# Kernel optimization log

Hardware: AMD Instinct MI355X
Metric: run time of the kernel (lower is better)

The kernel has to match this reference:

```python
import jax, jax.numpy as jnp
import numpy as np
import math

# irreps: 512x0 + 512x1 + 512x2 + 512x3 + 512x4 (SO3), mul_ir layout
LS = [0, 1, 2, 3, 4]
MULS = [512, 512, 512, 512, 512]
LMAX = 4
N = 4096
DIM = sum(m * (2 * l + 1) for m, l in zip(MULS, LS))  # 12800


def _small_d(l, beta):
    """Complex Wigner small-d matrix d^l_{m',m}(beta), m ordered -l..l (numpy, static)."""
    d = np.zeros((2 * l + 1, 2 * l + 1))
    cb, sb = math.cos(beta / 2.0), math.sin(beta / 2.0)
    for i, mp in enumerate(range(-l, l + 1)):
        for j, m in enumerate(range(-l, l + 1)):
            num = math.sqrt(math.factorial(l + mp) * math.factorial(l - mp)
                            * math.factorial(l + m) * math.factorial(l - m))
            tot = 0.0
            for s in range(max(0, m - mp), min(l + m, l - mp) + 1):
                den = (math.factorial(l + m - s) * math.factorial(s)
                       * math.factorial(mp - m + s) * math.factorial(l - mp - s))
                tot += ((-1.0) ** (mp - m + s)) * num / den \
                       * cb ** (2 * l + m - mp - 2 * s) * sb ** (mp - m + 2 * s)
            d[i, j] = tot
    return d


def _real_basis(l):
    """Unitary complex->real spherical-harmonic change of basis A (rows: real m=-l..l)."""
    A = np.zeros((2 * l + 1, 2 * l + 1), dtype=complex)
    A[l, l] = 1.0
    inv_s2 = 1.0 / math.sqrt(2.0)
    for m in range(1, l + 1):
        A[l + m, l + m] = ((-1) ** m) * inv_s2
        A[l + m, l - m] = inv_s2
        A[l - m, l + m] = -1j * ((-1) ** m) * inv_s2
        A[l - m, l - m] = 1j * inv_s2
    return A


def _J(l):
    """Real Wigner-D of the +pi/2 rotation that maps the 'easy' axis onto x.
    Conjugating the closed-form easy-axis rotation by J gives the x-axis rotation."""
    A = _real_basis(l)
    Dc = _small_d(l, math.pi / 2.0).astype(complex)
    return np.real(A @ Dc @ A.conj().T).astype(np.float32)


_JS = {l: _J(l) for l in LS if l > 0}


def _encode(angle, lmax):
    """[cos(l a), ..., cos(a), 1, sin(a), ..., sin(l a)] exactly as encode_rotation_angle."""
    m = jnp.arange(1, lmax + 1, dtype=angle.dtype)
    a = angle[:, None]
    c = jnp.cos(m * a)
    s = jnp.sin(m * a)
    return jnp.concatenate([c[:, ::-1], jnp.ones_like(a), s], axis=-1)  # [N, 2*lmax+1]


def _easy(enc, l, lmax):
    """Per-sample easy-axis rotation matrix for degree l built from the angle encoding.
    Rows/cols ordered m = -l..l: diag cos(|m|a), antidiag -sin(m a)."""
    d = 2 * l + 1
    m = np.arange(-l, l + 1)
    sign = np.sign(m).astype(np.float32)
    cos_v = enc[:, lmax - np.abs(m)]                 # [N, d] cos(|m| a)
    sin_v = enc[:, lmax + np.abs(m)] * sign          # [N, d] sin(m a)
    i = np.arange(d)
    E = jnp.zeros((enc.shape[0], d, d), enc.dtype)
    E = E.at[:, i, i].set(cos_v)
    E = E.at[:, i, d - 1 - i].add(-sin_v)            # add: center (m=0) overlaps diag, sin(0)=0
    return E


def _rotate(gamma, beta, alpha, x):
    n = x.shape[0]
    eg = _encode(gamma, LMAX)
    eb = _encode(beta, LMAX)
    ea = _encode(alpha, LMAX)
    outs = []
    off = 0
    for mul, l in zip(MULS, LS):
        d = 2 * l + 1
        seg = x[:, off:off + mul * d].reshape(n, mul, d)
        off += mul * d
        if l == 0:
            outs.append(seg.reshape(n, mul))  # scalars are rotation-invariant
            continue
        J = jnp.asarray(_JS[l], dtype=x.dtype)
        Eg = _easy(eg, l, LMAX)
        Eb = _easy(eb, l, LMAX)
        Ea = _easy(ea, l, LMAX)
        # yxy rotation: D = E(alpha) . J . E(beta) . J^T . E(gamma)
        D = Ea @ jnp.matmul(J, Eb @ jnp.matmul(J.T, Eg))  # [N, d, d]
        outs.append(jnp.einsum('nij,nuj->nui', D, seg).reshape(n, mul * d))
    return jnp.concatenate(outs, axis=-1)


def setup_inputs() -> dict:
    key = jax.random.key(0)
    kg, kb, ka, kx = jax.random.split(key, 4)
    pi = math.pi
    return {
        'gamma': jax.random.uniform(kg, (N,), jnp.float32, -pi, pi),
        'beta': jax.random.uniform(kb, (N,), jnp.float32, -pi, pi),
        'alpha': jax.random.uniform(ka, (N,), jnp.float32, -pi, pi),
        'x': jax.random.normal(kx, (N, DIM), jnp.float32),
    }


def reference(gamma, beta, alpha, x):
    return _rotate(gamma, beta, alpha, x)
```

## Files before the change

### kernel.cpp

```cpp
#include <hip/hip_runtime.h>
#include <math.h>

#define NSAMP 4096
#define DIMX  12800

#define JTOT 164

__global__ __launch_bounds__(256) void initJ_kernel(float* __restrict__ Jout) {
    __shared__ double dm[JTOT];
    __shared__ double Ar[JTOT], Ai[JTOT];
    __shared__ double Br[JTOT], Bi[JTOT];

    const int tid = threadIdx.x;
    int l = 0, base = 0, d = 0, ii = 0, jj = 0;
    const bool act = tid < JTOT;
    if (act) {
        if (tid < 9)       { l = 1; base = 0; }
        else if (tid < 34) { l = 2; base = 9; }
        else if (tid < 83) { l = 3; base = 34; }
        else               { l = 4; base = 83; }
        d = 2 * l + 1;
        int loc = tid - base;
        ii = loc / d;
        jj = loc - ii * d;

        double fact[9];
        fact[0] = 1.0;
        for (int k = 1; k < 9; k++) fact[k] = fact[k - 1] * (double)k;

        const int mp = ii - l, m = jj - l;
        const double num = sqrt(fact[l + mp] * fact[l - mp] * fact[l + m] * fact[l - m]);
        const double c2 = 0.70710678118654752440;
        double tot = 0.0;
        const int s0 = (m - mp > 0) ? (m - mp) : 0;
        const int s1 = (l + m < l - mp) ? (l + m) : (l - mp);
        for (int s = s0; s <= s1; s++) {
            double den = fact[l + m - s] * fact[s] * fact[mp - m + s] * fact[l - mp - s];
            int etot = (2 * l + m - mp - 2 * s) + (mp - m + 2 * s);
            double p = 1.0;
            for (int q = 0; q < etot; q++) p *= c2;
            double sgn = ((mp - m + s) & 1) ? -1.0 : 1.0;
            tot += sgn * (num / den) * p;
        }
        dm[tid] = tot;

        double ar = 0.0, ai = 0.0;
        const double inv_s2 = 0.70710678118654752440;
        if (ii == l) {
            if (jj == l) ar = 1.0;
        } else if (ii > l) {
            int mm = ii - l;
            if (jj == l + mm)      ar = (mm & 1) ? -inv_s2 : inv_s2;
            else if (jj == l - mm) ar = inv_s2;
        } else {
            int mm = l - ii;
            if (jj == l + mm)      ai = (mm & 1) ? inv_s2 : -inv_s2;
            else if (jj == l - mm) ai = inv_s2;
        }
        Ar[tid] = ar; Ai[tid] = ai;
    }
    __syncthreads();
    if (act) {
        double br = 0.0, bi = 0.0;
        for (int k = 0; k < d; k++) {
            double dv = dm[base + k * d + jj];
            br += Ar[base + ii * d + k] * dv;
            bi += Ai[base + ii * d + k] * dv;
        }
        Br[tid] = br; Bi[tid] = bi;
    }
    __syncthreads();
    if (act) {
        double jr = 0.0;
        for (int k = 0; k < d; k++) {
            jr += Br[base + ii * d + k] * Ar[base + jj * d + k]
                + Bi[base + ii * d + k] * Ai[base + jj * d + k];
        }
        Jout[tid] = (float)jr;
    }
}

template <int L>
__device__ __forceinline__ void apply_l(const float* __restrict__ xs_base,
                                        float* __restrict__ os_base,
                                        const float* __restrict__ Dl, int tid) {
    constexpr int d = 2 * L + 1;
#pragma unroll
    for (int rep = 0; rep < 2; rep++) {
        const int g = tid + rep * 256;
        const float* xs = xs_base + g * d;
        float v[d];
#pragma unroll
        for (int j = 0; j < d; j++) v[j] = xs[j];
        float r[d];
#pragma unroll
        for (int i = 0; i < d; i++) {
            float acc = 0.0f;
#pragma unroll
            for (int j = 0; j < d; j++) acc = fmaf(Dl[i * d + j], v[j], acc);
            r[i] = acc;
        }
        float* os = os_base + g * d;
#pragma unroll
        for (int i = 0; i < d; i++) os[i] = r[i];
    }
}

__global__ __launch_bounds__(256) void rot_main(
    const float* __restrict__ gamma, const float* __restrict__ beta,
    const float* __restrict__ alpha, const float* __restrict__ x,
    const float* __restrict__ Jws, float* __restrict__ out) {
    __shared__ float sJ[JTOT];
    __shared__ float sD[JTOT];
    __shared__ float sT0[JTOT];
    __shared__ float sT1[JTOT];
    __shared__ float trig[3][10];

    const int tid = threadIdx.x;
    const int n = blockIdx.x;

    if (tid < JTOT) sJ[tid] = Jws[tid];
    if (tid < 30) {
        int ai = tid / 10, k = tid % 10;
        float ang = (ai == 0) ? gamma[n] : (ai == 1) ? beta[n] : alpha[n];
        trig[ai][k] = (k < 5) ? cosf((float)k * ang) : sinf((float)(k - 5) * ang);
    }
    __syncthreads();

    int l = 0, base = 0, d = 0, ii = 0, jj = 0;
    const bool act = tid < JTOT;
    if (act) {
        if (tid < 9)       { l = 1; base = 0; }
        else if (tid < 34) { l = 2; base = 9; }
        else if (tid < 83) { l = 3; base = 34; }
        else               { l = 4; base = 83; }
        d = 2 * l + 1;
        int loc = tid - base;
        ii = loc / d;
        jj = loc - ii * d;
    }
    if (act) {
        int am = jj - l, aa = (am < 0) ? -am : am;
        float cv = trig[0][aa];
        float sv = (am > 0) ? trig[0][5 + aa] : (am < 0) ? -trig[0][5 + aa] : 0.0f;
        sT0[tid] = sJ[base + jj * d + ii] * cv + sJ[base + (d - 1 - jj) * d + ii] * sv;
    }
    __syncthreads();
    if (act) {
        int am = ii - l, aa = (am < 0) ? -am : am;
        float cv = trig[1][aa];
        float sv = (am > 0) ? trig[1][5 + aa] : (am < 0) ? -trig[1][5 + aa] : 0.0f;
        sT1[tid] = cv * sT0[tid] - sv * sT0[base + (d - 1 - ii) * d + jj];
    }
    __syncthreads();
    if (act) {
        float acc = 0.0f;
        for (int k = 0; k < d; k++)
            acc = fmaf(sJ[base + ii * d + k], sT1[base + k * d + jj], acc);
        sT0[tid] = acc;
    }
    __syncthreads();
    if (act) {
        int am = ii - l, aa = (am < 0) ? -am : am;
        float cv = trig[2][aa];
        float sv = (am > 0) ? trig[2][5 + aa] : (am < 0) ? -trig[2][5 + aa] : 0.0f;
        sD[tid] = cv * sT0[tid] - sv * sT0[base + (d - 1 - ii) * d + jj];
    }
    __syncthreads();

    const float* xrow = x + (size_t)n * DIMX;
    float* orow = out + (size_t)n * DIMX;

    {
        const float2* xv = (const float2*)xrow;
        float2* ov = (float2*)orow;
        ov[tid] = xv[tid];
    }
    apply_l<1>(xrow + 512,  orow + 512,  &sD[0],  tid);
    apply_l<2>(xrow + 2048, orow + 2048, &sD[9],  tid);
    apply_l<3>(xrow + 4608, orow + 4608, &sD[34], tid);
    apply_l<4>(xrow + 8192, orow + 8192, &sD[83], tid);
}

extern "C" void kernel_launch(void* const* d_in, const int* in_sizes, int n_in,
                              void* d_out, int out_size, void* d_ws, size_t ws_size,
                              hipStream_t stream) {
    const float* gamma = (const float*)d_in[0];
    const float* beta  = (const float*)d_in[1];
    const float* alpha = (const float*)d_in[2];
    const float* x     = (const float*)d_in[3];
    float* out = (float*)d_out;
    float* Jws = (float*)d_ws;

    hipLaunchKernelGGL(initJ_kernel, dim3(1), dim3(256), 0, stream, Jws);
    hipLaunchKernelGGL(rot_main, dim3(NSAMP), dim3(256), 0, stream,
                       gamma, beta, alpha, x, Jws, out);
}
```

Measured before the change: 362.5 us.

## Stage per-degree x segments through LDS with coalesced float4 copies

```diff
diff --git a/kernel.cpp b/kernel.cpp
--- a/kernel.cpp
+++ b/kernel.cpp
@@ -80,19 +80,17 @@
     }
 }
 
-template <int L>
-__device__ __forceinline__ void apply_l(const float* __restrict__ xs_base,
-                                        float* __restrict__ os_base,
-                                        const float* __restrict__ Dl, int tid) {
-    constexpr int d = 2 * L + 1;
+template <int d>
+__device__ __forceinline__ void compute_groups(float* __restrict__ sx,
+                                               const float* __restrict__ Dl,
+                                               int tid) {
 #pragma unroll
     for (int rep = 0; rep < 2; rep++) {
         const int g = tid + rep * 256;
-        const float* xs = xs_base + g * d;
-        float v[d];
-#pragma unroll
-        for (int j = 0; j < d; j++) v[j] = xs[j];
-        float r[d];
+        float* p = sx + g * d;
+        float v[d], r[d];
+#pragma unroll
+        for (int j = 0; j < d; j++) v[j] = p[j];
 #pragma unroll
         for (int i = 0; i < d; i++) {
             float acc = 0.0f;
@@ -100,10 +98,19 @@
             for (int j = 0; j < d; j++) acc = fmaf(Dl[i * d + j], v[j], acc);
             r[i] = acc;
         }
-        float* os = os_base + g * d;
-#pragma unroll
-        for (int i = 0; i < d; i++) os[i] = r[i];
-    }
+#pragma unroll
+        for (int i = 0; i < d; i++) p[i] = r[i];
+    }
+}
+
+__device__ __forceinline__ void lds_load(const float4* __restrict__ src,
+                                         float4* __restrict__ dst, int nf4, int tid) {
+    for (int i = tid; i < nf4; i += 256) dst[i] = src[i];
+}
+
+__device__ __forceinline__ void lds_store(float4* __restrict__ dst,
+                                          const float4* __restrict__ src, int nf4, int tid) {
+    for (int i = tid; i < nf4; i += 256) dst[i] = src[i];
 }
 
 __global__ __launch_bounds__(256) void rot_main(
@@ -115,9 +122,20 @@
     __shared__ float sT0[JTOT];
     __shared__ float sT1[JTOT];
     __shared__ float trig[3][10];
+    __shared__ __align__(16) float sx[4608];
+    float4* sx4 = (float4*)sx;
 
     const int tid = threadIdx.x;
     const int n = blockIdx.x;
+
+    const float* xrow = x + (size_t)n * DIMX;
+    float* orow = out + (size_t)n * DIMX;
+    const float4* xrow4 = (const float4*)xrow;
+    float4* orow4 = (float4*)orow;
+
+    if (tid < 128) orow4[tid] = xrow4[tid];
+
+    lds_load(xrow4 + 128, sx4, 384, tid);
 
     if (tid < JTOT) sJ[tid] = Jws[tid];
     if (tid < 30) {
@@ -168,18 +186,27 @@
     }
     __syncthreads();
 
-    const float* xrow = x + (size_t)n * DIMX;
-    float* orow = out + (size_t)n * DIMX;
-
-    {
-        const float2* xv = (const float2*)xrow;
-        float2* ov = (float2*)orow;
-        ov[tid] = xv[tid];
-    }
-    apply_l<1>(xrow + 512,  orow + 512,  &sD[0],  tid);
-    apply_l<2>(xrow + 2048, orow + 2048, &sD[9],  tid);
-    apply_l<3>(xrow + 4608, orow + 4608, &sD[34], tid);
-    apply_l<4>(xrow + 8192, orow + 8192, &sD[83], tid);
+    compute_groups<3>(sx, &sD[0], tid);
+    __syncthreads();
+    lds_store(orow4 + 128, sx4, 384, tid);
+    __syncthreads();
+    lds_load(xrow4 + 512, sx4, 640, tid);
+    __syncthreads();
+    compute_groups<5>(sx, &sD[9], tid);
+    __syncthreads();
+    lds_store(orow4 + 512, sx4, 640, tid);
+    __syncthreads();
+    lds_load(xrow4 + 1152, sx4, 896, tid);
+    __syncthreads();
+    compute_groups<7>(sx, &sD[34], tid);
+    __syncthreads();
+    lds_store(orow4 + 1152, sx4, 896, tid);
+    __syncthreads();
+    lds_load(xrow4 + 2048, sx4, 1152, tid);
+    __syncthreads();
+    compute_groups<9>(sx, &sD[83], tid);
+    __syncthreads();
+    lds_store(orow4 + 2048, sx4, 1152, tid);
 }
 
 extern "C" void kernel_launch(void* const* d_in, const int* in_sizes, int n_in,
```

Result: no change. 365.3 us (+0.8%).
